# Optimization experiments

Measured on AMD Instinct MI355X. Metric: run time of the kernel, lower is better.

The kernel has to match this reference:

```python
import jax, jax.numpy as jnp
import numpy as np

N_PTS, C = 500000, 16
B, R, SR, K = 1, 4096, 128, 8
N = R * SR  # total sampled points


def setup_inputs() -> dict:
    key = jax.random.key(0)
    ks = jax.random.split(key, 7)
    points_feat = jax.random.normal(ks[0], (N_PTS, C), dtype=jnp.float32)
    indices = jax.random.randint(ks[1], (B, N, K), 0, N_PTS)
    dists = jax.random.uniform(ks[2], (B, N, K), minval=0.01, maxval=1.0, dtype=jnp.float32)
    w_rgb = jax.random.normal(ks[3], (C, 3), dtype=jnp.float32) * 0.1
    w_sigma = jax.random.normal(ks[4], (C, 1), dtype=jnp.float32) * 0.1
    delta = jax.random.uniform(ks[5], (B, R, SR), minval=0.001, maxval=0.05, dtype=jnp.float32)
    z_vals = jnp.sort(jax.random.uniform(ks[6], (B, R, SR), minval=2.0, maxval=6.0, dtype=jnp.float32), axis=-1)
    return {"points_feat": points_feat, "indices": indices, "dists": dists,
            "w_rgb": w_rgb, "w_sigma": w_sigma, "delta": delta, "z_vals": z_vals}


def reference(points_feat, indices, dists, w_rgb, w_sigma, delta, z_vals):
    # --- neighbor_search weighting: inverse-distance weights, normalized over K ---
    w = 1.0 / (dists + 1e-7)                    # [B, N, K]
    w = w / jnp.sum(w, axis=-1, keepdims=True)
    # --- KNN feature gather + weighted aggregation (segment-reduce over K) ---
    gathered = points_feat[indices]             # [B, N, K, C]
    feat = jnp.einsum('bnk,bnkc->bnc', w, gathered)  # [B, N, C]
    # --- small head to radiance / density (stand-in for neural_points.forward) ---
    rgb = jax.nn.sigmoid(feat @ w_rgb).reshape(B, R, SR, 3)
    sigma = jax.nn.relu((feat @ w_sigma)[..., 0]).reshape(B, R, SR)
    # --- raw2output: per-ray volumetric alpha compositing ---
    alpha = 1.0 - jnp.exp(-sigma * delta)       # [B, R, SR]
    trans = jnp.cumprod(1.0 - alpha + 1e-10, axis=-1)
    trans = jnp.concatenate([jnp.ones_like(trans[..., :1]), trans[..., :-1]], axis=-1)
    wts = alpha * trans                          # [B, R, SR]
    rgb_map = jnp.einsum('brs,brsc->brc', wts, rgb)   # [B, R, 3]
    depth_map = jnp.sum(wts * z_vals, axis=-1)        # [B, R]
    acc_map = jnp.sum(wts, axis=-1)                   # [B, R]
    rgb_map = rgb_map + (1.0 - acc_map)[..., None]    # white background
    return jnp.concatenate([rgb_map, depth_map[..., None], acc_map[..., None]], axis=-1)  # [B, R, 5]
```

## Files before the change

### kernel.cpp

```cpp
#include <hip/hip_runtime.h>
#include <hip/hip_fp16.h>
#include <math.h>

#define KNN 8
#define CF 16
#define SRS 128
#define NRAYS 4096
#define TPB 128

__global__ __launch_bounds__(256) void hproj_kernel(
    const float* __restrict__ pf,
    const float* __restrict__ w_rgb,
    const float* __restrict__ w_sigma,
    uint2* __restrict__ hproj, int npts)
{
    const int p = blockIdx.x * blockDim.x + threadIdx.x;
    if (p >= npts) return;
    const float4* r4 = (const float4*)(pf + (long long)p * CF);
    const float4 a = r4[0], b = r4[1], c = r4[2], d = r4[3];
    const float f[CF] = {a.x, a.y, a.z, a.w, b.x, b.y, b.z, b.w,
                         c.x, c.y, c.z, c.w, d.x, d.y, d.z, d.w};
    float h0 = 0.f, h1 = 0.f, h2 = 0.f, h3 = 0.f;
#pragma unroll
    for (int k = 0; k < CF; ++k) {
        const float fc = f[k];
        h0 = fmaf(fc, w_rgb[k * 3 + 0], h0);
        h1 = fmaf(fc, w_rgb[k * 3 + 1], h1);
        h2 = fmaf(fc, w_rgb[k * 3 + 2], h2);
        h3 = fmaf(fc, w_sigma[k], h3);
    }
    union { __half2 h[2]; uint2 u; } pk;
    pk.h[0] = __floats2half2_rn(h0, h1);
    pk.h[1] = __floats2half2_rn(h2, h3);
    hproj[p] = pk.u;
}

__global__ __launch_bounds__(TPB) void pvr_main(
    const uint2* __restrict__ hproj,
    const int*   __restrict__ indices,
    const float* __restrict__ dists,
    const float* __restrict__ delta,
    const float* __restrict__ z_vals,
    float* __restrict__ out)
{
    const int ray  = blockIdx.x;
    const int t    = threadIdx.x;
    const int lane = t & 63;
    const int wid  = t >> 6;
    const long long n = (long long)ray * SRS + t;

    __shared__ float s_wavetot;
    __shared__ float s_red[2][5];

    const unsigned long long* ip = (const unsigned long long*)(indices + n * KNN);
    const unsigned long long* dp = (const unsigned long long*)(dists + n * KNN);
    unsigned long long iu[4], du[4];
#pragma unroll
    for (int m = 0; m < 4; ++m) {
        iu[m] = __builtin_nontemporal_load(ip + m);
        du[m] = __builtin_nontemporal_load(dp + m);
    }

    int   idx[KNN];
    float wk[KNN];
#pragma unroll
    for (int m = 0; m < 4; ++m) {
        idx[2 * m]     = (int)(iu[m] & 0xffffffffull);
        idx[2 * m + 1] = (int)(iu[m] >> 32);
        const float dlo = __uint_as_float((unsigned)(du[m] & 0xffffffffull));
        const float dhi = __uint_as_float((unsigned)(du[m] >> 32));
        wk[2 * m]     = 1.0f / (dlo + 1e-7f);
        wk[2 * m + 1] = 1.0f / (dhi + 1e-7f);
    }
    float wsum = 0.f;
#pragma unroll
    for (int k = 0; k < KNN; ++k) wsum += wk[k];
    const float winv = 1.0f / wsum;

    uint2 g[KNN];
#pragma unroll
    for (int k = 0; k < KNN; ++k) g[k] = hproj[(unsigned)idx[k]];

    float h0 = 0.f, h1 = 0.f, h2 = 0.f, h3 = 0.f;
#pragma unroll
    for (int k = 0; k < KNN; ++k) {
        union { unsigned u; __half2 h; } c0, c1;
        c0.u = g[k].x; c1.u = g[k].y;
        const float2 lo = __half22float2(c0.h);
        const float2 hi = __half22float2(c1.h);
        h0 = fmaf(wk[k], lo.x, h0);
        h1 = fmaf(wk[k], lo.y, h1);
        h2 = fmaf(wk[k], hi.x, h2);
        h3 = fmaf(wk[k], hi.y, h3);
    }

    const float r0 = 1.0f / (1.0f + expf(-h0 * winv));
    const float r1 = 1.0f / (1.0f + expf(-h1 * winv));
    const float r2 = 1.0f / (1.0f + expf(-h2 * winv));
    const float sg = fmaxf(h3 * winv, 0.0f);

    const float del = __builtin_nontemporal_load(delta  + n);
    const float zv  = __builtin_nontemporal_load(z_vals + n);
    const float alpha = 1.0f - expf(-sg * del);

    float p = 1.0f - alpha + 1e-10f;
#pragma unroll
    for (int off = 1; off < 64; off <<= 1) {
        const float v = __shfl_up(p, off, 64);
        if (lane >= off) p *= v;
    }
    if (wid == 0 && lane == 63) s_wavetot = p;
    __syncthreads();

    const float pm1 = __shfl_up(p, 1, 64);
    float excl = (lane == 0) ? 1.0f : pm1;
    if (wid == 1) excl *= s_wavetot;
    const float wts = alpha * excl;

    float v0 = wts * r0;
    float v1 = wts * r1;
    float v2 = wts * r2;
    float v3 = wts * zv;
    float v4 = wts;
#pragma unroll
    for (int off = 32; off >= 1; off >>= 1) {
        v0 += __shfl_down(v0, off, 64);
        v1 += __shfl_down(v1, off, 64);
        v2 += __shfl_down(v2, off, 64);
        v3 += __shfl_down(v3, off, 64);
        v4 += __shfl_down(v4, off, 64);
    }
    if (lane == 0) {
        s_red[wid][0] = v0;
        s_red[wid][1] = v1;
        s_red[wid][2] = v2;
        s_red[wid][3] = v3;
        s_red[wid][4] = v4;
    }
    __syncthreads();

    if (t == 0) {
        const float q0  = s_red[0][0] + s_red[1][0];
        const float q1  = s_red[0][1] + s_red[1][1];
        const float q2  = s_red[0][2] + s_red[1][2];
        const float dep = s_red[0][3] + s_red[1][3];
        const float acc = s_red[0][4] + s_red[1][4];
        const float bg  = 1.0f - acc;
        float* o = out + (long long)ray * 5;
        o[0] = q0 + bg;
        o[1] = q1 + bg;
        o[2] = q2 + bg;
        o[3] = dep;
        o[4] = acc;
    }
}

__global__ __launch_bounds__(512) void pvr_fused_f32(
    const float* __restrict__ points_feat,
    const int*   __restrict__ indices,
    const float* __restrict__ dists,
    const float* __restrict__ w_rgb,
    const float* __restrict__ w_sigma,
    const float* __restrict__ delta,
    const float* __restrict__ z_vals,
    float* __restrict__ out)
{
    const int ray = blockIdx.x;
    const int t   = threadIdx.x;
    const int s   = t >> 2;
    const int j   = t & 3;
    const long long n = (long long)ray * SRS + s;

    __shared__ float s_wrgb[CF * 3];
    __shared__ float s_wsig[CF];
    __shared__ float s_sig[SRS];
    __shared__ float s_rgbv[3][SRS];
    __shared__ float s_wavetot;
    __shared__ float s_red[2][5];

    if (t < CF * 3)            s_wrgb[t] = w_rgb[t];
    else if (t < CF * 3 + CF)  s_wsig[t - CF * 3] = w_sigma[t - CF * 3];

    const int2   i2 = ((const int2*)indices)[n * 4 + j];
    const float2 d2 = ((const float2*)dists)[n * 4 + j];

    float w0 = 1.0f / (d2.x + 1e-7f);
    float w1 = 1.0f / (d2.y + 1e-7f);
    float wsum = w0 + w1;
    wsum += __shfl_xor(wsum, 1);
    wsum += __shfl_xor(wsum, 2);
    const float winv = 1.0f / wsum;

    int   idxk[KNN];
    float wk[KNN];
#pragma unroll
    for (int m = 0; m < 4; ++m) {
        idxk[2 * m]     = __shfl(i2.x, m, 4);
        idxk[2 * m + 1] = __shfl(i2.y, m, 4);
        wk[2 * m]       = __shfl(w0, m, 4);
        wk[2 * m + 1]   = __shfl(w1, m, 4);
    }

    const float4* pf4 = (const float4*)points_feat;
    float4 r[KNN];
#pragma unroll
    for (int k = 0; k < KNN; ++k)
        r[k] = pf4[(long long)idxk[k] * 4 + j];

    float4 f = make_float4(0.f, 0.f, 0.f, 0.f);
#pragma unroll
    for (int k = 0; k < KNN; ++k) {
        f.x = fmaf(wk[k], r[k].x, f.x);
        f.y = fmaf(wk[k], r[k].y, f.y);
        f.z = fmaf(wk[k], r[k].z, f.z);
        f.w = fmaf(wk[k], r[k].w, f.w);
    }

    __syncthreads();

    float pr0 = 0.f, pr1 = 0.f, pr2 = 0.f, ps = 0.f;
    {
        const float fv[4] = {f.x, f.y, f.z, f.w};
#pragma unroll
        for (int m = 0; m < 4; ++m) {
            const int c = 4 * j + m;
            pr0 = fmaf(fv[m], s_wrgb[c * 3 + 0], pr0);
            pr1 = fmaf(fv[m], s_wrgb[c * 3 + 1], pr1);
            pr2 = fmaf(fv[m], s_wrgb[c * 3 + 2], pr2);
            ps  = fmaf(fv[m], s_wsig[c], ps);
        }
    }
    pr0 += __shfl_xor(pr0, 1); pr0 += __shfl_xor(pr0, 2);
    pr1 += __shfl_xor(pr1, 1); pr1 += __shfl_xor(pr1, 2);
    pr2 += __shfl_xor(pr2, 1); pr2 += __shfl_xor(pr2, 2);
    ps  += __shfl_xor(ps, 1);  ps  += __shfl_xor(ps, 2);

    if (j == 0) {
        s_sig[s]     = ps * winv;
        s_rgbv[0][s] = 1.0f / (1.0f + expf(-pr0 * winv));
        s_rgbv[1][s] = 1.0f / (1.0f + expf(-pr1 * winv));
        s_rgbv[2][s] = 1.0f / (1.0f + expf(-pr2 * winv));
    }
    __syncthreads();

    float p = 0.0f, alpha = 0.0f, zv = 0.0f;
    float r0 = 0.0f, r1 = 0.0f, r2 = 0.0f;
    const int lane = t & 63;
    const int wid  = t >> 6;
    if (t < SRS) {
        const long long m = (long long)ray * SRS + t;
        const float del = __builtin_nontemporal_load(delta  + m);
        zv              = __builtin_nontemporal_load(z_vals + m);
        const float sg  = fmaxf(s_sig[t], 0.0f);
        alpha = 1.0f - expf(-sg * del);
        r0 = s_rgbv[0][t]; r1 = s_rgbv[1][t]; r2 = s_rgbv[2][t];

        p = 1.0f - alpha + 1e-10f;
#pragma unroll
        for (int off = 1; off < 64; off <<= 1) {
            float v = __shfl_up(p, off, 64);
            if (lane >= off) p *= v;
        }
        if (wid == 0 && lane == 63) s_wavetot = p;
    }
    __syncthreads();

    if (t < SRS) {
        float pm1  = __shfl_up(p, 1, 64);
        float excl = (lane == 0) ? 1.0f : pm1;
        if (wid == 1) excl *= s_wavetot;
        const float wts = alpha * excl;

        float v0 = wts * r0;
        float v1 = wts * r1;
        float v2 = wts * r2;
        float v3 = wts * zv;
        float v4 = wts;
#pragma unroll
        for (int off = 32; off >= 1; off >>= 1) {
            v0 += __shfl_down(v0, off, 64);
            v1 += __shfl_down(v1, off, 64);
            v2 += __shfl_down(v2, off, 64);
            v3 += __shfl_down(v3, off, 64);
            v4 += __shfl_down(v4, off, 64);
        }
        if (lane == 0) {
            s_red[wid][0] = v0;
            s_red[wid][1] = v1;
            s_red[wid][2] = v2;
            s_red[wid][3] = v3;
            s_red[wid][4] = v4;
        }
    }
    __syncthreads();

    if (t == 0) {
        float q0  = s_red[0][0] + s_red[1][0];
        float q1  = s_red[0][1] + s_red[1][1];
        float q2  = s_red[0][2] + s_red[1][2];
        float dep = s_red[0][3] + s_red[1][3];
        float acc = s_red[0][4] + s_red[1][4];
        float bg  = 1.0f - acc;
        float* o = out + (long long)ray * 5;
        o[0] = q0 + bg;
        o[1] = q1 + bg;
        o[2] = q2 + bg;
        o[3] = dep;
        o[4] = acc;
    }
}

extern "C" void kernel_launch(void* const* d_in, const int* in_sizes, int n_in,
                              void* d_out, int out_size, void* d_ws, size_t ws_size,
                              hipStream_t stream) {
    const float* points_feat = (const float*)d_in[0];
    const int*   indices     = (const int*)d_in[1];
    const float* dists       = (const float*)d_in[2];
    const float* w_rgb       = (const float*)d_in[3];
    const float* w_sigma     = (const float*)d_in[4];
    const float* delta       = (const float*)d_in[5];
    const float* z_vals      = (const float*)d_in[6];
    float* out = (float*)d_out;

    const int npts = in_sizes[0] / CF;
    const size_t need = (size_t)npts * sizeof(uint2);
    if (ws_size >= need) {
        hproj_kernel<<<(npts + 255) / 256, 256, 0, stream>>>(
            points_feat, w_rgb, w_sigma, (uint2*)d_ws, npts);
        pvr_main<<<NRAYS, TPB, 0, stream>>>(
            (const uint2*)d_ws, indices, dists, delta, z_vals, out);
    } else {
        pvr_fused_f32<<<NRAYS, 512, 0, stream>>>(
            points_feat, indices, dists, w_rgb, w_sigma, delta, z_vals, out);
    }
}
```

Before: 42.59 us.

## Split fused ray kernel into separate gather and compositing kernels

The fused per-ray kernel is split in two. A flat gather kernel with 256-thread blocks does the KNN gather, weighting, head and alpha, and writes a float4 per sample to workspace. A separate per-ray compositing kernel then does the scan and reduction. The aim is to free the latency-bound random gathers from the per-ray scan and its block barriers so occupancy is higher, at the cost of an extra kernel launch and a round trip of about 8 MB through memory. It also needs more workspace, and if that is not available the code falls back to the slow fp32 path.

```diff
diff --git a/kernel.cpp b/kernel.cpp
--- a/kernel.cpp
+++ b/kernel.cpp
@@ -6,7 +6,9 @@
 #define CF 16
 #define SRS 128
 #define NRAYS 4096
-#define TPB 128
+#define NSAMP (NRAYS * SRS)
+
+typedef unsigned long long u64;
 
 __global__ __launch_bounds__(256) void hproj_kernel(
     const float* __restrict__ pf,
@@ -35,51 +37,46 @@
     hproj[p] = pk.u;
 }
 
-__global__ __launch_bounds__(TPB) void pvr_main(
+__global__ __launch_bounds__(256) void gather_kernel(
     const uint2* __restrict__ hproj,
     const int*   __restrict__ indices,
     const float* __restrict__ dists,
     const float* __restrict__ delta,
-    const float* __restrict__ z_vals,
-    float* __restrict__ out)
+    float4* __restrict__ smp)
 {
-    const int ray  = blockIdx.x;
-    const int t    = threadIdx.x;
-    const int lane = t & 63;
-    const int wid  = t >> 6;
-    const long long n = (long long)ray * SRS + t;
-
-    __shared__ float s_wavetot;
-    __shared__ float s_red[2][5];
-
-    const unsigned long long* ip = (const unsigned long long*)(indices + n * KNN);
-    const unsigned long long* dp = (const unsigned long long*)(dists + n * KNN);
-    unsigned long long iu[4], du[4];
+    const int n = blockIdx.x * blockDim.x + threadIdx.x;
+    if (n >= NSAMP) return;
+
+    const u64* ip = (const u64*)(indices + (long long)n * KNN);
+    const u64* dp = (const u64*)(dists   + (long long)n * KNN);
+    u64 iu[4], du[4];
 #pragma unroll
     for (int m = 0; m < 4; ++m) {
         iu[m] = __builtin_nontemporal_load(ip + m);
         du[m] = __builtin_nontemporal_load(dp + m);
     }
-
-    int   idx[KNN];
-    float wk[KNN];
+    const float del = __builtin_nontemporal_load(delta + n);
+
+    int idx[KNN];
 #pragma unroll
     for (int m = 0; m < 4; ++m) {
         idx[2 * m]     = (int)(iu[m] & 0xffffffffull);
         idx[2 * m + 1] = (int)(iu[m] >> 32);
-        const float dlo = __uint_as_float((unsigned)(du[m] & 0xffffffffull));
-        const float dhi = __uint_as_float((unsigned)(du[m] >> 32));
-        wk[2 * m]     = 1.0f / (dlo + 1e-7f);
-        wk[2 * m + 1] = 1.0f / (dhi + 1e-7f);
+    }
+    uint2 g[KNN];
+#pragma unroll
+    for (int k = 0; k < KNN; ++k) g[k] = hproj[(unsigned)idx[k]];
+
+    float wk[KNN];
+#pragma unroll
+    for (int m = 0; m < 4; ++m) {
+        wk[2 * m]     = 1.0f / (__uint_as_float((unsigned)(du[m] & 0xffffffffull)) + 1e-7f);
+        wk[2 * m + 1] = 1.0f / (__uint_as_float((unsigned)(du[m] >> 32)) + 1e-7f);
     }
     float wsum = 0.f;
 #pragma unroll
     for (int k = 0; k < KNN; ++k) wsum += wk[k];
     const float winv = 1.0f / wsum;
-
-    uint2 g[KNN];
-#pragma unroll
-    for (int k = 0; k < KNN; ++k) g[k] = hproj[(unsigned)idx[k]];
 
     float h0 = 0.f, h1 = 0.f, h2 = 0.f, h3 = 0.f;
 #pragma unroll
@@ -94,20 +91,38 @@
         h3 = fmaf(wk[k], hi.y, h3);
     }
 
-    const float r0 = 1.0f / (1.0f + expf(-h0 * winv));
-    const float r1 = 1.0f / (1.0f + expf(-h1 * winv));
-    const float r2 = 1.0f / (1.0f + expf(-h2 * winv));
+    float4 o;
+    o.x = 1.0f / (1.0f + expf(-h0 * winv));
+    o.y = 1.0f / (1.0f + expf(-h1 * winv));
+    o.z = 1.0f / (1.0f + expf(-h2 * winv));
     const float sg = fmaxf(h3 * winv, 0.0f);
-
-    const float del = __builtin_nontemporal_load(delta  + n);
-    const float zv  = __builtin_nontemporal_load(z_vals + n);
-    const float alpha = 1.0f - expf(-sg * del);
+    o.w = 1.0f - expf(-sg * del);
+    smp[n] = o;
+}
+
+__global__ __launch_bounds__(SRS) void composite_kernel(
+    const float4* __restrict__ smp,
+    const float*  __restrict__ z_vals,
+    float* __restrict__ out)
+{
+    const int ray  = blockIdx.x;
+    const int t    = threadIdx.x;
+    const int lane = t & 63;
+    const int wid  = t >> 6;
+    const long long n = (long long)ray * SRS + t;
+
+    __shared__ float s_wavetot;
+    __shared__ float s_red[2][5];
+
+    const float4 v  = smp[n];
+    const float  zv = __builtin_nontemporal_load(z_vals + n);
+    const float alpha = v.w;
 
     float p = 1.0f - alpha + 1e-10f;
 #pragma unroll
     for (int off = 1; off < 64; off <<= 1) {
-        const float v = __shfl_up(p, off, 64);
-        if (lane >= off) p *= v;
+        const float u = __shfl_up(p, off, 64);
+        if (lane >= off) p *= u;
     }
     if (wid == 0 && lane == 63) s_wavetot = p;
     __syncthreads();
@@ -117,9 +132,9 @@
     if (wid == 1) excl *= s_wavetot;
     const float wts = alpha * excl;
 
-    float v0 = wts * r0;
-    float v1 = wts * r1;
-    float v2 = wts * r2;
+    float v0 = wts * v.x;
+    float v1 = wts * v.y;
+    float v2 = wts * v.z;
     float v3 = wts * zv;
     float v4 = wts;
 #pragma unroll
@@ -323,12 +338,16 @@
     float* out = (float*)d_out;
 
     const int npts = in_sizes[0] / CF;
-    const size_t need = (size_t)npts * sizeof(uint2);
-    if (ws_size >= need) {
+    const size_t tbl_bytes = (size_t)npts * sizeof(uint2);
+    const size_t smp_bytes = (size_t)NSAMP * sizeof(float4);
+    if (ws_size >= tbl_bytes + smp_bytes) {
+        uint2*  tbl = (uint2*)d_ws;
+        float4* smp = (float4*)((char*)d_ws + tbl_bytes);
         hproj_kernel<<<(npts + 255) / 256, 256, 0, stream>>>(
-            points_feat, w_rgb, w_sigma, (uint2*)d_ws, npts);
-        pvr_main<<<NRAYS, TPB, 0, stream>>>(
-            (const uint2*)d_ws, indices, dists, delta, z_vals, out);
+            points_feat, w_rgb, w_sigma, tbl, npts);
+        gather_kernel<<<(NSAMP + 255) / 256, 256, 0, stream>>>(
+            tbl, indices, dists, delta, smp);
+        composite_kernel<<<NRAYS, SRS, 0, stream>>>(smp, z_vals, out);
     } else {
         pvr_fused_f32<<<NRAYS, 512, 0, stream>>>(
             points_feat, indices, dists, w_rgb, w_sigma, delta, z_vals, out);
```

New measurement: 48.64 us. 1.14x slower.
